# Kernel tuning notes

Hardware: AMD Instinct MI355X
Metric: run time of the kernel (lower is better)

Reference implementation:

```python
import jax, jax.numpy as jnp
import numpy as np

H = 8
D = 512
DK = D // H  # 64
ALPHA = 0.2  # leaky relu negative slope


def setup_inputs() -> dict:
    key = jax.random.key(0)
    ks = jax.random.split(key, 10)
    B, N = 8, 1024
    query = jax.random.normal(ks[0], (B, N, D), dtype=jnp.float32)
    key_t = jax.random.normal(ks[1], (B, N, D), dtype=jnp.float32)
    value = jax.random.normal(ks[2], (B, N, D), dtype=jnp.float32)
    mask = jax.random.randint(ks[3], (B, N, N), 0, 2, dtype=jnp.int32)
    scale = 0.02
    Wq = jax.random.normal(ks[4], (D, D), dtype=jnp.float32) * scale
    Wk = jax.random.normal(ks[5], (D, D), dtype=jnp.float32) * scale
    Wv = jax.random.normal(ks[6], (D, D), dtype=jnp.float32) * scale
    Wo = jax.random.normal(ks[7], (D, D), dtype=jnp.float32) * scale
    bq = jnp.zeros((D,), jnp.float32)
    bk = jnp.zeros((D,), jnp.float32)
    bv = jnp.zeros((D,), jnp.float32)
    bo = jnp.zeros((D,), jnp.float32)
    # xavier-uniform-like init for the attention vector a: shape (h, 2*d_k)
    limit = float(np.sqrt(6.0 / (H + 2 * DK)))
    a = jax.random.uniform(ks[8], (H, 2 * DK), dtype=jnp.float32, minval=-limit, maxval=limit)
    return {"query": query, "key": key_t, "value": value, "mask": mask,
            "Wq": Wq, "bq": bq, "Wk": Wk, "bk": bk, "Wv": Wv, "bv": bv,
            "Wo": Wo, "bo": bo, "a": a}


def reference(query, key, value, mask, Wq, bq, Wk, bk, Wv, bv, Wo, bo, a):
    B, N, _ = query.shape

    def proj(x, W, b):
        # torch Linear: x @ W.T + b, then split heads -> (B, H, N, DK)
        return (x @ W.T + b).reshape(B, N, H, DK).transpose(0, 2, 1, 3)

    q = proj(query, Wq, bq)
    k = proj(key, Wk, bk)
    v = proj(value, Wv, bv)

    # 'cat' attention: scores[b,h,i,j] = concat(q_i, k_j) . a[h]
    #                = q_i . a[h,:DK] + k_j . a[h,DK:]  (algebraic decomposition,
    #                 avoids the O(N^2 * 2*DK) concat tensor of the torch code)
    sq = jnp.einsum('bhnd,hd->bhn', q, a[:, :DK])
    sk = jnp.einsum('bhnd,hd->bhn', k, a[:, DK:])
    scores = sq[:, :, :, None] + sk[:, :, None, :]  # (B, H, N, N)

    # mask == 0 -> -inf (mask broadcast over heads), applied BEFORE leaky relu
    scores = jnp.where(mask[:, None, :, :] == 0, -jnp.inf, scores)
    # leaky relu (leaky_relu(-inf) == -inf, preserved)
    scores = jnp.where(scores >= 0, scores, ALPHA * scores)

    p = jax.nn.softmax(scores, axis=-1)
    # fully-masked rows produce NaN -> replace with 0 (as in the torch code)
    p = jnp.where(jnp.isnan(p), jnp.zeros_like(p), p)

    x = jnp.einsum('bhnm,bhmd->bhnd', p, v)
    x = x.transpose(0, 2, 1, 3).reshape(B, N, D)
    return x @ Wo.T + bo
```

## Files before the change

kernel.cpp:

```cpp
#include <hip/hip_runtime.h>
#include <hip/hip_bf16.h>
#include <stdint.h>


typedef __attribute__((ext_vector_type(8))) short short8;
typedef __attribute__((ext_vector_type(4))) float f32x4;

#define LB __launch_bounds__(256)

union U8 { unsigned u[4]; short8 s; uint4 v; };
union U2 { unsigned u[2]; uint2 v; };

__device__ __forceinline__ unsigned short f2bf(float f) {
  unsigned int u = __float_as_uint(f);
  u += 0x7fffu + ((u >> 16) & 1u);
  return (unsigned short)(u >> 16);
}

__device__ __forceinline__ unsigned cvt_pk(float a, float b) {
  unsigned r;
  asm("v_cvt_pk_bf16_f32 %0, %1, %2" : "=v"(r) : "v"(a), "v"(b));
  return r;
}

__device__ __forceinline__ void async_cp16(const void* g, void* l) {
  __builtin_amdgcn_global_load_lds(
      (const __attribute__((address_space(1))) unsigned int*)g,
      (__attribute__((address_space(3))) unsigned int*)l, 16, 0, 0);
}

__global__ LB void prep_kernel(const float* __restrict__ Wv, const float* __restrict__ Wo,
                               unsigned short* __restrict__ wv16, unsigned short* __restrict__ wo16,
                               const float* __restrict__ Wq, const float* __restrict__ Wk,
                               const float* __restrict__ a, const float* __restrict__ bq,
                               const float* __restrict__ bk,
                               unsigned short* __restrict__ Bfrag, float* __restrict__ qkb) {
  const int blk = blockIdx.x, tid = threadIdx.x;
  if (blk < 512) {
    const float* src = blk < 256 ? Wv : Wo;
    unsigned short* dst = blk < 256 ? wv16 : wo16;
    const int idx = ((blk & 255) * 256 + tid) * 4;
    const float4 v = *(const float4*)(src + idx);
    U2 pk;
    pk.u[0] = cvt_pk(v.x, v.y);
    pk.u[1] = cvt_pk(v.z, v.w);
    *(uint2*)(dst + idx) = pk.v;
    return;
  }
  const int t = (blk - 512) * 256 + tid;
  const int d = t & 511, h = t >> 9;
  float aq = 0.f, ak = 0.f;
#pragma unroll 4
  for (int dk = 0; dk < 64; ++dk) {
    aq += Wq[(size_t)(h * 64 + dk) * 512 + d] * a[h * 128 + dk];
    ak += Wk[(size_t)(h * 64 + dk) * 512 + d] * a[h * 128 + 64 + dk];
  }
  const float L2E = 1.4426950408889634f;
  const int ks = d >> 5, lch = (d >> 3) & 3, tt = d & 7;
  Bfrag[((ks * 64 + (lch << 4) + h) << 3) + tt] = f2bf(aq * L2E);
  Bfrag[((ks * 64 + (lch << 4) + 8 + h) << 3) + tt] = f2bf(ak * L2E);
  if (d == 0) {
    float s1 = 0.f, s2 = 0.f;
    for (int dk = 0; dk < 64; ++dk) {
      s1 += bq[h * 64 + dk] * a[h * 128 + dk];
      s2 += bk[h * 64 + dk] * a[h * 128 + 64 + dk];
    }
    qkb[h] = s1 * L2E;
    qkb[8 + h] = s2 * L2E;
  }
}

__global__ LB void mid_kernel(const float* __restrict__ query, const float* __restrict__ key,
                              const unsigned short* __restrict__ Bfrag,
                              const float* __restrict__ qkb,
                              float2* __restrict__ sqE, float2* __restrict__ skE,
                              const float* __restrict__ value,
                              const unsigned short* __restrict__ wv16,
                              const float* __restrict__ bvb, unsigned short* __restrict__ vt,
                              const int* __restrict__ mask, unsigned int* __restrict__ bits) {
  __shared__ char sm[20480];
  const int tid = threadIdx.x, w = tid >> 6, l = tid & 63;
  const int lr = l & 15, lc = l >> 4;
  const int bid = blockIdx.x;
  if (bid >= 1536) {
    unsigned char* nb = (unsigned char*)sm;
    const size_t e0 = ((size_t)(bid - 1536) * 256 + tid) * 4;
    const int4 m = *(const int4*)(mask + e0);
    nb[tid] = (unsigned char)((m.x != 0) | ((m.y != 0) << 1) | ((m.z != 0) << 2) | ((m.w != 0) << 3));
    __syncthreads();
    if (tid < 32) {
      const uint2 p = *(const uint2*)(nb + tid * 8);
      const unsigned lo = p.x, hi = p.y;
      const unsigned wl = (lo & 0xFu) | ((lo >> 4) & 0xF0u) | ((lo >> 8) & 0xF00u) | ((lo >> 12) & 0xF000u);
      const unsigned wh = (hi & 0xFu) | ((hi >> 4) & 0xF0u) | ((hi >> 8) & 0xF00u) | ((hi >> 12) & 0xF000u);
      bits[(bid - 1536) * 32 + tid] = wl | (wh << 16);
    }
    return;
  }
  if (bid >= 1024) {
    float* comb = (float*)sm;
    const int m0 = (bid - 1024) * 16;
    const int k0 = w * 128;
    short8 bf[4];
#pragma unroll
    for (int ks = 0; ks < 4; ++ks)
      bf[ks] = *(const short8*)(Bfrag + (((w * 4 + ks) * 64 + l) << 3));
    const float* qbase = query + (size_t)(m0 + lr) * 512 + k0 + (lc << 3);
    const float* kbase = key + (size_t)(m0 + lr) * 512 + k0 + (lc << 3);
    f32x4 cq = {}, ck = {};
#pragma unroll
    for (int ks = 0; ks < 4; ++ks) {
      const float4 q0 = *(const float4*)(qbase + ks * 32);
      const float4 q1 = *(const float4*)(qbase + ks * 32 + 4);
      const float4 k0v = *(const float4*)(kbase + ks * 32);
      const float4 k1v = *(const float4*)(kbase + ks * 32 + 4);
      U8 aq, ak;
      aq.u[0] = cvt_pk(q0.x, q0.y); aq.u[1] = cvt_pk(q0.z, q0.w);
      aq.u[2] = cvt_pk(q1.x, q1.y); aq.u[3] = cvt_pk(q1.z, q1.w);
      ak.u[0] = cvt_pk(k0v.x, k0v.y); ak.u[1] = cvt_pk(k0v.z, k0v.w);
      ak.u[2] = cvt_pk(k1v.x, k1v.y); ak.u[3] = cvt_pk(k1v.z, k1v.w);
      cq = __builtin_amdgcn_mfma_f32_16x16x32_bf16(aq.s, bf[ks], cq, 0, 0, 0);
      ck = __builtin_amdgcn_mfma_f32_16x16x32_bf16(ak.s, bf[ks], ck, 0, 0, 0);
    }
    if (w) {
      float* p = comb + ((w - 1) * 64 + l) * 9;
#pragma unroll
      for (int r = 0; r < 4; ++r) { p[r] = cq[r]; p[4 + r] = ck[r]; }
    }
    __syncthreads();
    if (w == 0) {
#pragma unroll
      for (int j = 0; j < 3; ++j) {
        const float* p = comb + (j * 64 + l) * 9;
#pragma unroll
        for (int r = 0; r < 4; ++r) { cq[r] += p[r]; ck[r] += p[4 + r]; }
      }
      const int col = l & 15;
      const int mbase = m0 + (lc << 2);
      const int b = mbase >> 10;
      const float bia = qkb[col];
      if (col < 8) {
        float2* out = sqE + ((size_t)b * 8 + col) * 1024;
#pragma unroll
        for (int r = 0; r < 4; ++r) {
          const float v = cq[r] + bia;
          float2 pr;
          pr.x = __builtin_amdgcn_exp2f(v);
          pr.y = __builtin_amdgcn_exp2f(0.2f * v);
          out[(mbase + r) & 1023] = pr;
        }
      } else {
        float2* out = skE + ((size_t)b * 8 + (col - 8)) * 1024;
#pragma unroll
        for (int r = 0; r < 4; ++r) {
          const float v = ck[r] + bia;
          float2 pr;
          pr.x = __builtin_amdgcn_exp2f(v);
          pr.y = __builtin_amdgcn_exp2f(0.2f * v);
          out[(mbase + r) & 1023] = pr;
        }
      }
    }
    return;
  }
  unsigned short* As = (unsigned short*)sm;
  unsigned short* Bs = (unsigned short*)(sm + 4096);
  const int bm = bid >> 2, bn = bid & 3;
  const int m0 = bm * 32, n0 = bn * 128;
  const int wr = (w & 1) * 16, wc = (w >> 1) * 64;
  const int rch = (lc ^ ((lr >> 1) & 3)) << 3;
  const int arow = (w << 3) + (l >> 3);
  const int akc = l & 7;
  const float* asrc = value + (size_t)(m0 + arow) * 512 + (akc << 2);
  const int ach = ((akc >> 1) ^ ((arow >> 1) & 3));
  const int aoff = arow * 32 + (ach << 3) + ((akc & 1) << 2);
  const int crow = l >> 2;
  const int brow0 = (w << 4) + crow, brow1 = ((w + 4) << 4) + crow;
  const unsigned short* bsrc0 = wv16 + (size_t)(n0 + brow0) * 512 + (((l & 3) ^ ((brow0 >> 1) & 3)) << 3);
  const unsigned short* bsrc1 = wv16 + (size_t)(n0 + brow1) * 512 + (((l & 3) ^ ((brow1 >> 1) & 3)) << 3);

  f32x4 acc[4] = {};
  float4 areg = *(const float4*)(asrc);
  async_cp16(bsrc0, Bs + (w << 9));
  async_cp16(bsrc1, Bs + ((w + 4) << 9));
  {
    U2 aw;
    aw.u[0] = cvt_pk(areg.x, areg.y);
    aw.u[1] = cvt_pk(areg.z, areg.w);
    *(uint2*)(As + aoff) = aw.v;
  }
  areg = *(const float4*)(asrc + 32);
  async_cp16(bsrc0 + 32, Bs + 4096 + (w << 9));
  async_cp16(bsrc1 + 32, Bs + 4096 + ((w + 4) << 9));
  asm volatile("s_waitcnt vmcnt(3)" ::: "memory");
  asm volatile("s_waitcnt lgkmcnt(0)" ::: "memory");
  __builtin_amdgcn_sched_barrier(0);
  __builtin_amdgcn_s_barrier();
  int buf = 0;
  for (int kt = 0; kt < 16; ++kt) {
    const short8 af = *(const short8*)(As + (buf << 10) + (wr + lr) * 32 + rch);
    __builtin_amdgcn_s_setprio(1);
#pragma unroll
    for (int j = 0; j < 4; ++j) {
      const short8 bfr = *(const short8*)(Bs + (buf << 12) + (wc + j * 16 + lr) * 32 + rch);
      acc[j] = __builtin_amdgcn_mfma_f32_16x16x32_bf16(af, bfr, acc[j], 0, 0, 0);
    }
    __builtin_amdgcn_s_setprio(0);
    __builtin_amdgcn_s_barrier();
    if (kt < 15) {
      U2 aw;
      aw.u[0] = cvt_pk(areg.x, areg.y);
      aw.u[1] = cvt_pk(areg.z, areg.w);
      *(uint2*)(As + ((buf ^ 1) << 10) + aoff) = aw.v;
      if (kt < 14) {
        areg = *(const float4*)(asrc + (kt + 2) * 32);
        async_cp16(bsrc0 + (kt + 2) * 32, Bs + (buf << 12) + (w << 9));
        async_cp16(bsrc1 + (kt + 2) * 32, Bs + (buf << 12) + ((w + 4) << 9));
        asm volatile("s_waitcnt vmcnt(3)" ::: "memory");
      } else {
        asm volatile("s_waitcnt vmcnt(0)" ::: "memory");
      }
      asm volatile("s_waitcnt lgkmcnt(0)" ::: "memory");
      __builtin_amdgcn_sched_barrier(0);
      __builtin_amdgcn_s_barrier();
    }
    buf ^= 1;
  }
#pragma unroll
  for (int j = 0; j < 4; ++j) {
    const int nn = n0 + wc + j * 16 + lr;
    const float bia = bvb[nn];
    const int mm0 = m0 + wr + lc * 4;
    const int b = mm0 >> 10, t0 = mm0 & 1023;
    const int h = nn >> 6, dk = nn & 63;
    U2 pk;
    pk.u[0] = cvt_pk(acc[j][0] + bia, acc[j][1] + bia);
    pk.u[1] = cvt_pk(acc[j][2] + bia, acc[j][3] + bia);
    *(uint2*)(vt + (((size_t)((b * 8 + h) * 64 + dk)) << 10) + t0) = pk.v;
  }
}

template <int BB16>
__global__ LB void gemm_bt(const unsigned short* __restrict__ A,
                           const void* __restrict__ Bwp,
                           const float* __restrict__ bias, float* __restrict__ outp) {
  __shared__ unsigned short As[2][32 * 32];
  __shared__ unsigned short Bs[2][128 * 32];
  const int tid = threadIdx.x;
  const int w = tid >> 6, l = tid & 63;
  const int lr = l & 15, lc = l >> 4;
  const int bm = blockIdx.x >> 2, bn = blockIdx.x & 3;
  const int m0 = bm * 32, n0 = bn * 128;
  const int wr = (w & 1) * 16, wc = (w >> 1) * 64;
  const int rch = (lc ^ ((lr >> 1) & 3)) << 3;
  const int arow = (w << 3) + (l >> 2);
  const int asc = (l & 3) ^ ((arow >> 1) & 3);
  const unsigned short* asrc = A + (size_t)(m0 + arow) * 512 + (asc << 3);
  const int crow = l >> 2;
  const unsigned short* b16 = (const unsigned short*)Bwp;
  const float* b32 = (const float*)Bwp;
  const int brow0 = (w << 4) + crow, brow1 = ((w + 4) << 4) + crow;
  const unsigned short* bsrc0 = b16 + (size_t)(n0 + brow0) * 512 + (((l & 3) ^ ((brow0 >> 1) & 3)) << 3);
  const unsigned short* bsrc1 = b16 + (size_t)(n0 + brow1) * 512 + (((l & 3) ^ ((brow1 >> 1) & 3)) << 3);

  f32x4 acc[4] = {};
  if (BB16) {
    if (l < 32) async_cp16(asrc, As[0] + (w << 8));
    async_cp16(bsrc0, Bs[0] + (w << 9));
    async_cp16(bsrc1, Bs[0] + ((w + 4) << 9));
    int buf = 0;
    for (int kt = 0; kt < 16; ++kt) {
      if (kt < 15) {
        const int k1 = (kt + 1) * 32;
        if (l < 32) async_cp16(asrc + k1, As[buf ^ 1] + (w << 8));
        async_cp16(bsrc0 + k1, Bs[buf ^ 1] + (w << 9));
        async_cp16(bsrc1 + k1, Bs[buf ^ 1] + ((w + 4) << 9));
        asm volatile("s_waitcnt vmcnt(3)" ::: "memory");
      } else {
        asm volatile("s_waitcnt vmcnt(0)" ::: "memory");
      }
      __builtin_amdgcn_sched_barrier(0);
      __builtin_amdgcn_s_barrier();
      const short8 af = *(const short8*)(As[buf] + (wr + lr) * 32 + rch);
      __builtin_amdgcn_s_setprio(1);
#pragma unroll
      for (int j = 0; j < 4; ++j) {
        const short8 bfr = *(const short8*)(Bs[buf] + (wc + j * 16 + lr) * 32 + rch);
        acc[j] = __builtin_amdgcn_mfma_f32_16x16x32_bf16(af, bfr, acc[j], 0, 0, 0);
      }
      __builtin_amdgcn_s_setprio(0);
      if (kt < 15) __builtin_amdgcn_s_barrier();
      buf ^= 1;
    }
  } else {
    for (int kt = 0; kt < 16; ++kt) {
      const int k0 = kt * 32;
      if (kt) __syncthreads();
      if (l < 32) async_cp16(asrc + k0, As[0] + (w << 8));
#pragma unroll
      for (int it = 0; it < 2; ++it) {
        const int idx = it * 256 + tid;
        const int row = idx >> 2, gr = idx & 3;
        const int sch = (gr ^ ((row >> 1) & 3)) << 3;
        const float4* src = (const float4*)(b32 + (size_t)(n0 + row) * 512 + k0 + gr * 8);
        const float4 b0 = src[0], b1 = src[1];
        U8 t8;
        t8.u[0] = cvt_pk(b0.x, b0.y); t8.u[1] = cvt_pk(b0.z, b0.w);
        t8.u[2] = cvt_pk(b1.x, b1.y); t8.u[3] = cvt_pk(b1.z, b1.w);
        *(uint4*)(Bs[0] + row * 32 + sch) = t8.v;
      }
      __syncthreads();
      const short8 af = *(const short8*)(As[0] + (wr + lr) * 32 + rch);
#pragma unroll
      for (int j = 0; j < 4; ++j) {
        const short8 bfr = *(const short8*)(Bs[0] + (wc + j * 16 + lr) * 32 + rch);
        acc[j] = __builtin_amdgcn_mfma_f32_16x16x32_bf16(af, bfr, acc[j], 0, 0, 0);
      }
    }
  }
#pragma unroll
  for (int j = 0; j < 4; ++j) {
    const int nn = n0 + wc + j * 16 + lr;
    const float bia = bias[nn];
    const int mm0 = m0 + wr + lc * 4;
#pragma unroll
    for (int r = 0; r < 4; ++r)
      outp[(size_t)(mm0 + r) * 512 + nn] = acc[j][r] + bia;
  }
}

__global__ LB void attn_kernel(const float2* __restrict__ sqE, const float2* __restrict__ skE,
                               const unsigned char* __restrict__ mbits,
                               const unsigned short* __restrict__ vt,
                               unsigned short* __restrict__ xb) {
  __shared__ char smem[57344];
  unsigned short* vts = (unsigned short*)smem;
  float* sksE = (float*)(smem + 32768);
  char* mks = smem + 40960;
  const int tid = threadIdx.x;
  const int w = tid >> 6, l = tid & 63;
  const int lr = l & 15, lc = l >> 4;
  const int bid = blockIdx.x;
  const int bh = bid & 63, iblk = bid >> 6;
  const int b = bh >> 3, h = bh & 7;
  const int i0b = iblk << 7;
  const int rh = w & 1, jh = w >> 1;
  const int j0 = jh << 9;
  const float* sqEp = (const float*)(sqE + (size_t)bh * 1024);
  const float* skEp = (const float*)(skE + (size_t)bh * 1024);
  const unsigned short* vtp = vt + ((size_t)bh << 16);
  const unsigned char* mrow = mbits + ((size_t)b << 17);

  async_cp16(skEp + (w << 9) + l * 4, sksE + (w << 9));
  async_cp16(skEp + (w << 9) + 256 + l * 4, sksE + (w << 9) + 256);
#pragma unroll
  for (int m = 0; m < 4; ++m) {
    const int row = (w << 5) + (m << 3) + (l >> 3);
    const int c = (l & 7) ^ (row & 7);
    async_cp16(mrow + (size_t)(i0b + row) * 128 + (c << 4), mks + (w << 12) + (m << 10));
  }
  const int sdk = l >> 3;
  const int c0 = (l & 7) ^ sdk;
  const unsigned short* vsA = vtp + (size_t)((rh << 5) + sdk) * 1024 + j0 + (c0 << 3);
  const unsigned short* vsB = vtp + (size_t)((rh << 5) + sdk) * 1024 + j0 + ((c0 ^ 4) << 3);
  unsigned short* vdst = vts + (jh << 13) + ((rh << 5) << 6);
#define STAGE(bf_, jsl_)                                                       \
  {                                                                            \
    unsigned short* d_ = vdst + ((bf_) << 12);                                 \
    async_cp16(vsA + (jsl_), d_);                                              \
    async_cp16(vsB + 8192 + (jsl_), d_ + 512);                                 \
    async_cp16(vsA + 16384 + (jsl_), d_ + 1024);                               \
    async_cp16(vsB + 24576 + (jsl_), d_ + 1536);                               \
  }
  STAGE(0, 0);
  float2 E8[4];
#pragma unroll
  for (int t = 0; t < 4; ++t)
    E8[t] = *(const float2*)(sqEp + ((i0b + (rh << 6) + (t << 4) + lr) << 1));
  __syncthreads();

  f32x4 acc[4][4] = {};
  f32x4 accs[4] = {};
  short8 ones;
#pragma unroll
  for (int t = 0; t < 8; ++t) ones[t] = (short)0x3f80;
  const int rx = (lr & 7) << 4;
  const int pxor = (lr & 7) ^ (((lr >> 3) & 1) << 2);

  int buf = 0;
  for (int slab = 0; slab < 8; ++slab) {
    if (slab < 7) {
      STAGE(buf ^ 1, (slab + 1) << 6);
      asm volatile("s_waitcnt vmcnt(4)" ::: "memory");
    } else {
      asm volatile("s_waitcnt vmcnt(0)" ::: "memory");
    }
    __builtin_amdgcn_sched_barrier(0);
    __builtin_amdgcn_s_barrier();
#pragma unroll
    for (int s2 = 0; s2 < 2; ++s2) {
      const int jb = j0 + (slab << 6) + (s2 << 5);
      const int qb = (jb >> 3) + lc;
      const float* sp = sksE + ((jb + (lc << 3)) << 1);
      const f32x4 q0 = *(const f32x4*)(sp);
      const f32x4 q1 = *(const f32x4*)(sp + 4);
      const f32x4 q2 = *(const f32x4*)(sp + 8);
      const f32x4 q3 = *(const f32x4*)(sp + 12);
      U8 pa[4];
#pragma unroll
      for (int t = 0; t < 4; ++t) {
        const int row = (rh << 6) + (t << 4) + lr;
        const unsigned mb = (unsigned char)mks[(row << 7) + (qb ^ rx)];
        const float Eq = E8[t].x, eq = E8[t].y;
        float e[8];
        e[0] = fmaxf(Eq * q0[0], eq * q0[1]); e[1] = fmaxf(Eq * q0[2], eq * q0[3]);
        e[2] = fmaxf(Eq * q1[0], eq * q1[1]); e[3] = fmaxf(Eq * q1[2], eq * q1[3]);
        e[4] = fmaxf(Eq * q2[0], eq * q2[1]); e[5] = fmaxf(Eq * q2[2], eq * q2[3]);
        e[6] = fmaxf(Eq * q3[0], eq * q3[1]); e[7] = fmaxf(Eq * q3[2], eq * q3[3]);
#pragma unroll
        for (int u = 0; u < 8; ++u)
          e[u] = (mb & (1u << u)) ? e[u] : 0.0f;
        pa[t].u[0] = cvt_pk(e[0], e[1]); pa[t].u[1] = cvt_pk(e[2], e[3]);
        pa[t].u[2] = cvt_pk(e[4], e[5]); pa[t].u[3] = cvt_pk(e[6], e[7]);
      }
      const unsigned short* vbb = vts + (jh << 13) + (buf << 12)
                                + ((((s2 << 2) + lc) ^ pxor) << 3);
      __builtin_amdgcn_s_setprio(1);
#pragma unroll
      for (int c = 0; c < 4; ++c) {
        const short8 bv = *(const short8*)(vbb + (((c << 4) + lr) << 6));
#pragma unroll
        for (int t = 0; t < 4; ++t)
          acc[t][c] = __builtin_amdgcn_mfma_f32_16x16x32_bf16(pa[t].s, bv, acc[t][c], 0, 0, 0);
      }
#pragma unroll
      for (int t = 0; t < 4; ++t)
        accs[t] = __builtin_amdgcn_mfma_f32_16x16x32_bf16(pa[t].s, ones, accs[t], 0, 0, 0);
      __builtin_amdgcn_s_setprio(0);
    }
    if (slab < 7) __builtin_amdgcn_s_barrier();
    buf ^= 1;
  }
#undef STAGE

  __syncthreads();
  float* cmb = (float*)smem;
  if (jh == 1) {
    float* p = cmb + ((rh << 6) + l) * 84;
#pragma unroll
    for (int t = 0; t < 4; ++t) {
#pragma unroll
      for (int c = 0; c < 4; ++c) *(f32x4*)(p + (t * 4 + c) * 4) = acc[t][c];
      *(f32x4*)(p + 64 + t * 4) = accs[t];
    }
  }
  __syncthreads();
  if (jh == 0) {
    const float* p = cmb + ((rh << 6) + l) * 84;
#pragma unroll
    for (int t = 0; t < 4; ++t) {
#pragma unroll
      for (int c = 0; c < 4; ++c) {
        const f32x4 v = *(const f32x4*)(p + (t * 4 + c) * 4);
#pragma unroll
        for (int r = 0; r < 4; ++r) acc[t][c][r] += v[r];
      }
      const f32x4 vs = *(const f32x4*)(p + 64 + t * 4);
#pragma unroll
      for (int r = 0; r < 4; ++r) accs[t][r] += vs[r];
    }
#pragma unroll
    for (int t = 0; t < 4; ++t) {
#pragma unroll
      for (int r = 0; r < 4; ++r) {
        const float sv = accs[t][r];
        const float inv = sv > 0.0f ? 1.0f / sv : 0.0f;
        const int i = i0b + (rh << 6) + (t << 4) + (lc << 2) + r;
#pragma unroll
        for (int c = 0; c < 4; ++c)
          xb[(((size_t)(b * 1024 + i)) << 9) + h * 64 + (c << 4) + lr] =
              f2bf(acc[t][c][r] * inv);
      }
    }
  }
}

extern "C" void kernel_launch(void* const* d_in, const int* in_sizes, int n_in,
                              void* d_out, int out_size, void* d_ws, size_t ws_size,
                              hipStream_t stream) {
  const float* query = (const float*)d_in[0];
  const float* key   = (const float*)d_in[1];
  const float* value = (const float*)d_in[2];
  const int*   mask  = (const int*)d_in[3];
  const float* Wq = (const float*)d_in[4];
  const float* bq = (const float*)d_in[5];
  const float* Wk = (const float*)d_in[6];
  const float* bk = (const float*)d_in[7];
  const float* Wv = (const float*)d_in[8];
  const float* bv = (const float*)d_in[9];
  const float* Wo = (const float*)d_in[10];
  const float* bo = (const float*)d_in[11];
  const float* a  = (const float*)d_in[12];

  char* oc = (char*)d_out;
  unsigned short* vt = (unsigned short*)(oc + 0);
  unsigned int* mbits = (unsigned int*)(oc + 8388608);
  unsigned short* Bfrag = (unsigned short*)(oc + 9961472);
  float* qkb = (float*)(oc + 9977856);
  unsigned short* wv16 = (unsigned short*)(oc + 10485760);
  float2* sqE = (float2*)(oc + 11010048);
  float2* skE = (float2*)(oc + 11534336);
  unsigned short* wo16f = (unsigned short*)(oc + 12058624);
  unsigned short* xb = (unsigned short*)d_ws;

  const bool roomy = ws_size >= 8912896;
  unsigned short* wo16 = roomy ? (unsigned short*)((char*)d_ws + 8388608) : wo16f;

  prep_kernel<<<528, 256, 0, stream>>>(Wv, Wo, wv16, wo16, Wq, Wk, a, bq, bk, Bfrag, qkb);
  mid_kernel<<<9728, 256, 0, stream>>>(query, key, Bfrag, qkb, sqE, skE,
                                       value, wv16, bv, vt, mask, mbits);
  attn_kernel<<<512, 256, 0, stream>>>(sqE, skE, (const unsigned char*)mbits, vt, xb);
  if (roomy)
    gemm_bt<1><<<1024, 256, 0, stream>>>(xb, (const void*)wo16, bo, (float*)d_out);
  else
    gemm_bt<0><<<1024, 256, 0, stream>>>(xb, (const void*)Wo, bo, (float*)d_out);
}
```

Baseline: 77.71 us.

## Load V fragments directly from global into registers, shrink LDS footprint

The attention kernel stops staging V tiles through double-buffered shared memory and instead loads each wave's MFMA B-operand fragments straight from global memory into registers, prefetching the next 32-column step. This removes the per-slab barriers and cuts LDS from 56KB to 24KB, which could raise occupancy. The cross-wave reduction is serialized over the two row halves so it fits in the smaller buffer. The cost is that each wave now issues its own global loads with less coalescing, and V data that was shared through LDS is fetched redundantly by different waves via cache.

```diff
diff --git a/kernel.cpp b/kernel.cpp
--- a/kernel.cpp
+++ b/kernel.cpp
@@ -333,10 +333,9 @@
                                const unsigned char* __restrict__ mbits,
                                const unsigned short* __restrict__ vt,
                                unsigned short* __restrict__ xb) {
-  __shared__ char smem[57344];
-  unsigned short* vts = (unsigned short*)smem;
-  float* sksE = (float*)(smem + 32768);
-  char* mks = smem + 40960;
+  __shared__ char smem[24576];
+  float* sksE = (float*)smem;
+  char* mks = smem + 8192;
   const int tid = threadIdx.x;
   const int w = tid >> 6, l = tid & 63;
   const int lr = l & 15, lc = l >> 4;
@@ -359,20 +358,6 @@
     const int c = (l & 7) ^ (row & 7);
     async_cp16(mrow + (size_t)(i0b + row) * 128 + (c << 4), mks + (w << 12) + (m << 10));
   }
-  const int sdk = l >> 3;
-  const int c0 = (l & 7) ^ sdk;
-  const unsigned short* vsA = vtp + (size_t)((rh << 5) + sdk) * 1024 + j0 + (c0 << 3);
-  const unsigned short* vsB = vtp + (size_t)((rh << 5) + sdk) * 1024 + j0 + ((c0 ^ 4) << 3);
-  unsigned short* vdst = vts + (jh << 13) + ((rh << 5) << 6);
-#define STAGE(bf_, jsl_)                                                       \
-  {                                                                            \
-    unsigned short* d_ = vdst + ((bf_) << 12);                                 \
-    async_cp16(vsA + (jsl_), d_);                                              \
-    async_cp16(vsB + 8192 + (jsl_), d_ + 512);                                 \
-    async_cp16(vsA + 16384 + (jsl_), d_ + 1024);                               \
-    async_cp16(vsB + 24576 + (jsl_), d_ + 1536);                               \
-  }
-  STAGE(0, 0);
   float2 E8[4];
 #pragma unroll
   for (int t = 0; t < 4; ++t)
@@ -385,103 +370,100 @@
 #pragma unroll
   for (int t = 0; t < 8; ++t) ones[t] = (short)0x3f80;
   const int rx = (lr & 7) << 4;
-  const int pxor = (lr & 7) ^ (((lr >> 3) & 1) << 2);
-
-  int buf = 0;
-  for (int slab = 0; slab < 8; ++slab) {
-    if (slab < 7) {
-      STAGE(buf ^ 1, (slab + 1) << 6);
-      asm volatile("s_waitcnt vmcnt(4)" ::: "memory");
-    } else {
-      asm volatile("s_waitcnt vmcnt(0)" ::: "memory");
-    }
-    __builtin_amdgcn_sched_barrier(0);
-    __builtin_amdgcn_s_barrier();
-#pragma unroll
-    for (int s2 = 0; s2 < 2; ++s2) {
-      const int jb = j0 + (slab << 6) + (s2 << 5);
-      const int qb = (jb >> 3) + lc;
-      const float* sp = sksE + ((jb + (lc << 3)) << 1);
-      const f32x4 q0 = *(const f32x4*)(sp);
-      const f32x4 q1 = *(const f32x4*)(sp + 4);
-      const f32x4 q2 = *(const f32x4*)(sp + 8);
-      const f32x4 q3 = *(const f32x4*)(sp + 12);
-      U8 pa[4];
+
+  const unsigned short* vfr = vtp + (size_t)lr * 1024 + j0 + (lc << 3);
+  short8 bvc[4], bvn[4];
+#pragma unroll
+  for (int c = 0; c < 4; ++c)
+    bvc[c] = *(const short8*)(vfr + (c << 14));
+
+  for (int it = 0; it < 16; ++it) {
+    const int jb = j0 + (it << 5);
+    const int qb = (jb >> 3) + lc;
+    const float* sp = sksE + ((jb + (lc << 3)) << 1);
+    const f32x4 q0 = *(const f32x4*)(sp);
+    const f32x4 q1 = *(const f32x4*)(sp + 4);
+    const f32x4 q2 = *(const f32x4*)(sp + 8);
+    const f32x4 q3 = *(const f32x4*)(sp + 12);
+    if (it < 15) {
+#pragma unroll
+      for (int c = 0; c < 4; ++c)
+        bvn[c] = *(const short8*)(vfr + ((it + 1) << 5) + (c << 14));
+    }
+    U8 pa[4];
+#pragma unroll
+    for (int t = 0; t < 4; ++t) {
+      const int row = (rh << 6) + (t << 4) + lr;
+      const unsigned mb = (unsigned char)mks[(row << 7) + (qb ^ rx)];
+      const float Eq = E8[t].x, eq = E8[t].y;
+      float e[8];
+      e[0] = fmaxf(Eq * q0[0], eq * q0[1]); e[1] = fmaxf(Eq * q0[2], eq * q0[3]);
+      e[2] = fmaxf(Eq * q1[0], eq * q1[1]); e[3] = fmaxf(Eq * q1[2], eq * q1[3]);
+      e[4] = fmaxf(Eq * q2[0], eq * q2[1]); e[5] = fmaxf(Eq * q2[2], eq * q2[3]);
+      e[6] = fmaxf(Eq * q3[0], eq * q3[1]); e[7] = fmaxf(Eq * q3[2], eq * q3[3]);
+#pragma unroll
+      for (int u = 0; u < 8; ++u)
+        e[u] = (mb & (1u << u)) ? e[u] : 0.0f;
+      pa[t].u[0] = cvt_pk(e[0], e[1]); pa[t].u[1] = cvt_pk(e[2], e[3]);
+      pa[t].u[2] = cvt_pk(e[4], e[5]); pa[t].u[3] = cvt_pk(e[6], e[7]);
+    }
+    __builtin_amdgcn_s_setprio(1);
+#pragma unroll
+    for (int c = 0; c < 4; ++c)
+#pragma unroll
+      for (int t = 0; t < 4; ++t)
+        acc[t][c] = __builtin_amdgcn_mfma_f32_16x16x32_bf16(pa[t].s, bvc[c], acc[t][c], 0, 0, 0);
+#pragma unroll
+    for (int t = 0; t < 4; ++t)
+      accs[t] = __builtin_amdgcn_mfma_f32_16x16x32_bf16(pa[t].s, ones, accs[t], 0, 0, 0);
+    __builtin_amdgcn_s_setprio(0);
+#pragma unroll
+    for (int c = 0; c < 4; ++c) bvc[c] = bvn[c];
+  }
+
+  float* cmb = (float*)smem;
+  __syncthreads();
+#pragma unroll 1
+  for (int rr = 0; rr < 2; ++rr) {
+    if (jh == 1 && rh == rr) {
+      float* p = cmb + l * 81;
 #pragma unroll
       for (int t = 0; t < 4; ++t) {
-        const int row = (rh << 6) + (t << 4) + lr;
-        const unsigned mb = (unsigned char)mks[(row << 7) + (qb ^ rx)];
-        const float Eq = E8[t].x, eq = E8[t].y;
-        float e[8];
-        e[0] = fmaxf(Eq * q0[0], eq * q0[1]); e[1] = fmaxf(Eq * q0[2], eq * q0[3]);
-        e[2] = fmaxf(Eq * q1[0], eq * q1[1]); e[3] = fmaxf(Eq * q1[2], eq * q1[3]);
-        e[4] = fmaxf(Eq * q2[0], eq * q2[1]); e[5] = fmaxf(Eq * q2[2], eq * q2[3]);
-        e[6] = fmaxf(Eq * q3[0], eq * q3[1]); e[7] = fmaxf(Eq * q3[2], eq * q3[3]);
-#pragma unroll
-        for (int u = 0; u < 8; ++u)
-          e[u] = (mb & (1u << u)) ? e[u] : 0.0f;
-        pa[t].u[0] = cvt_pk(e[0], e[1]); pa[t].u[1] = cvt_pk(e[2], e[3]);
-        pa[t].u[2] = cvt_pk(e[4], e[5]); pa[t].u[3] = cvt_pk(e[6], e[7]);
-      }
-      const unsigned short* vbb = vts + (jh << 13) + (buf << 12)
-                                + ((((s2 << 2) + lc) ^ pxor) << 3);
-      __builtin_amdgcn_s_setprio(1);
-#pragma unroll
-      for (int c = 0; c < 4; ++c) {
-        const short8 bv = *(const short8*)(vbb + (((c << 4) + lr) << 6));
-#pragma unroll
-        for (int t = 0; t < 4; ++t)
-          acc[t][c] = __builtin_amdgcn_mfma_f32_16x16x32_bf16(pa[t].s, bv, acc[t][c], 0, 0, 0);
-      }
-#pragma unroll
-      for (int t = 0; t < 4; ++t)
-        accs[t] = __builtin_amdgcn_mfma_f32_16x16x32_bf16(pa[t].s, ones, accs[t], 0, 0, 0);
-      __builtin_amdgcn_s_setprio(0);
-    }
-    if (slab < 7) __builtin_amdgcn_s_barrier();
-    buf ^= 1;
-  }
-#undef STAGE
-
-  __syncthreads();
-  float* cmb = (float*)smem;
-  if (jh == 1) {
-    float* p = cmb + ((rh << 6) + l) * 84;
-#pragma unroll
-    for (int t = 0; t < 4; ++t) {
-#pragma unroll
-      for (int c = 0; c < 4; ++c) *(f32x4*)(p + (t * 4 + c) * 4) = acc[t][c];
-      *(f32x4*)(p + 64 + t * 4) = accs[t];
-    }
-  }
-  __syncthreads();
-  if (jh == 0) {
-    const float* p = cmb + ((rh << 6) + l) * 84;
-#pragma unroll
-    for (int t = 0; t < 4; ++t) {
-#pragma unroll
-      for (int c = 0; c < 4; ++c) {
-        const f32x4 v = *(const f32x4*)(p + (t * 4 + c) * 4);
-#pragma unroll
-        for (int r = 0; r < 4; ++r) acc[t][c][r] += v[r];
-      }
-      const f32x4 vs = *(const f32x4*)(p + 64 + t * 4);
-#pragma unroll
-      for (int r = 0; r < 4; ++r) accs[t][r] += vs[r];
-    }
-#pragma unroll
-    for (int t = 0; t < 4; ++t) {
-#pragma unroll
-      for (int r = 0; r < 4; ++r) {
-        const float sv = accs[t][r];
-        const float inv = sv > 0.0f ? 1.0f / sv : 0.0f;
-        const int i = i0b + (rh << 6) + (t << 4) + (lc << 2) + r;
-#pragma unroll
-        for (int c = 0; c < 4; ++c)
-          xb[(((size_t)(b * 1024 + i)) << 9) + h * 64 + (c << 4) + lr] =
-              f2bf(acc[t][c][r] * inv);
-      }
-    }
+#pragma unroll
+        for (int c = 0; c < 4; ++c) *(f32x4*)(p + (t * 4 + c) * 4) = acc[t][c];
+        *(f32x4*)(p + 64 + t * 4) = accs[t];
+      }
+    }
+    __syncthreads();
+    if (jh == 0 && rh == rr) {
+      const float* p = cmb + l * 81;
+#pragma unroll
+      for (int t = 0; t < 4; ++t) {
+#pragma unroll
+        for (int c = 0; c < 4; ++c) {
+          const f32x4 v = *(const f32x4*)(p + (t * 4 + c) * 4);
+#pragma unroll
+          for (int r = 0; r < 4; ++r) acc[t][c][r] += v[r];
+        }
+        const f32x4 vs = *(const f32x4*)(p + 64 + t * 4);
+#pragma unroll
+        for (int r = 0; r < 4; ++r) accs[t][r] += vs[r];
+      }
+#pragma unroll
+      for (int t = 0; t < 4; ++t) {
+#pragma unroll
+        for (int r = 0; r < 4; ++r) {
+          const float sv = accs[t][r];
+          const float inv = sv > 0.0f ? 1.0f / sv : 0.0f;
+          const int i = i0b + (rh << 6) + (t << 4) + (lc << 2) + r;
+#pragma unroll
+          for (int c = 0; c < 4; ++c)
+            xb[(((size_t)(b * 1024 + i)) << 9) + h * 64 + (c << 4) + lr] =
+                f2bf(acc[t][c][r] * inv);
+        }
+      }
+    }
+    __syncthreads();
   }
 }
 
```

After: 78.73 us. Within noise of the previous version (+1.3%).
